# Kernel optimization log

Hardware: AMD Instinct MI355X
Metric: run time of the kernel (lower is better)

Reference implementation:

```python
import jax, jax.numpy as jnp
import numpy as np

N = 262144  # points
C = 256     # backbone_out_channels
K = 20      # semantic_num_classes
BN_EPS = 1e-3
EPS = 1e-8
IGNORE = -1


def setup_inputs() -> dict:
    key = jax.random.key(0)
    ks = jax.random.split(key, 12)
    feat = jax.random.normal(ks[0], (N, C), dtype=jnp.float32)
    coord = jax.random.normal(ks[1], (N, 3), dtype=jnp.float32)
    instance_centroid = jax.random.normal(ks[2], (N, 3), dtype=jnp.float32)
    segment = jax.random.randint(ks[3], (N,), 0, K, dtype=jnp.int32)
    instance = jax.random.randint(ks[4], (N,), 0, 1000, dtype=jnp.int32)
    # bias_head: Linear(C,C) -> BN1d(C) -> ReLU -> Linear(C,3)
    w1 = jax.random.normal(ks[5], (C, C), dtype=jnp.float32) * 0.02
    b1 = jnp.zeros((C,), dtype=jnp.float32)
    gamma = jnp.ones((C,), dtype=jnp.float32)
    beta = jnp.zeros((C,), dtype=jnp.float32)
    w2 = jax.random.normal(ks[6], (C, 3), dtype=jnp.float32) * 0.02
    b2 = jnp.zeros((3,), dtype=jnp.float32)
    # seg_head: Linear(C, K)
    ws = jax.random.normal(ks[7], (C, K), dtype=jnp.float32) * 0.02
    bs = jnp.zeros((K,), dtype=jnp.float32)
    return dict(feat=feat, coord=coord, instance_centroid=instance_centroid,
                segment=segment, instance=instance,
                w1=w1, b1=b1, gamma=gamma, beta=beta, w2=w2, b2=b2, ws=ws, bs=bs)


def reference(feat, coord, instance_centroid, segment, instance,
              w1, b1, gamma, beta, w2, b2, ws, bs):
    # bias head: Linear -> BatchNorm1d (training stats) -> ReLU -> Linear
    h = feat @ w1 + b1                                  # [N, C]
    mu = jnp.mean(h, axis=0)
    var = jnp.mean((h - mu) ** 2, axis=0)               # biased var (torch BN)
    h = (h - mu) * jax.lax.rsqrt(var + BN_EPS) * gamma + beta
    h = jax.nn.relu(h)
    bias_pred = h @ w2 + b2                             # [N, 3]

    logit_pred = feat @ ws + bs                         # [N, K]

    # semantic cross-entropy with ignore_index
    valid = segment != IGNORE
    tgt = jnp.where(valid, segment, 0)
    logp = jax.nn.log_softmax(logit_pred, axis=-1)
    nll = -jnp.take_along_axis(logp, tgt[:, None], axis=1)[:, 0]
    vf = valid.astype(logit_pred.dtype)
    seg_loss = jnp.sum(nll * vf) / (jnp.sum(vf) + EPS)

    # masked bias L1 loss
    mask = (instance != IGNORE).astype(bias_pred.dtype)
    bias_gt = instance_centroid - coord                 # [N, 3]
    bias_dist = jnp.sum(jnp.abs(bias_pred - bias_gt), axis=-1)
    msum = jnp.sum(mask) + EPS
    bias_l1_loss = jnp.sum(bias_dist * mask) / msum

    # masked cosine (direction) loss
    pred_n = bias_pred / (jnp.linalg.norm(bias_pred, axis=1, keepdims=True) + EPS)
    gt_n = bias_gt / (jnp.linalg.norm(bias_gt, axis=1, keepdims=True) + EPS)
    cos = -jnp.sum(pred_n * gt_n, axis=-1)
    bias_cosine_loss = jnp.sum(cos * mask) / msum

    loss = seg_loss + bias_l1_loss + bias_cosine_loss
    return jnp.stack([loss, seg_loss, bias_l1_loss, bias_cosine_loss])
```

## Files before the change

### kernel.cpp

```cpp
#include <hip/hip_runtime.h>
#include <cstdio>
#include <cstdint>

typedef unsigned int u32;
typedef unsigned short u16;
typedef short bf16x8 __attribute__((ext_vector_type(8)));
typedef float f32x4 __attribute__((ext_vector_type(4)));

#define NPTS 262144
#define CDIM 256
#define KCLS 20
#define NBLK 4096
#define NSLOT 256
#define LSLOT 256

#define OFF_WT    ((size_t)134217728)
#define OFF_AGGBN (OFF_WT + (size_t)163840)
#define OFF_AGGNL (OFF_AGGBN + (size_t)524288)
#define OFF_AGGL  (OFF_AGGNL + (size_t)2048)
#define OFF_AB    (OFF_AGGL + (size_t)4096)
#define WS_NEED   (OFF_AB + (size_t)2048)
#define MEMSET_OFF OFF_AGGBN
#define MEMSET_LEN ((size_t)(524288 + 2048 + 4096))

__device__ __forceinline__ u16 bf16rne(float x) {
    u32 u = __float_as_uint(x);
    u32 r = u + 0x7FFFu + ((u >> 16) & 1u);
    return (u16)(r >> 16);
}
__device__ __forceinline__ float bf2f(u16 b) {
    return __uint_as_float(((u32)b) << 16);
}

__global__ void k_prep(const float* __restrict__ w1, const float* __restrict__ wsm,
                       u16* __restrict__ Wt) {
    int k = blockIdx.x;
    int n = threadIdx.x;
    float v = 0.f;
    if (n < 256) v = w1[k * 256 + n];
    else if (n < 256 + KCLS) v = wsm[k * KCLS + (n - 256)];
    Wt[n * 256 + k] = bf16rne(v);
}

__global__ __launch_bounds__(256) void k_gemm(
    const float* __restrict__ feat, const float* __restrict__ b1,
    const float* __restrict__ bs, const int* __restrict__ segment,
    const u16* __restrict__ Wt, u16* __restrict__ h_out,
    float* __restrict__ aggBN, float* __restrict__ aggNLL)
{
    __shared__ uint4 smem4[3072];
    uint4* const As4 = smem4;
    uint4* const Bs4 = smem4 + 512;

    const int t = threadIdx.x;
    const int lane = t & 63;
    const int wv = t >> 6;
    const int q = lane >> 4;
    const int i16 = lane & 15;
    const int row0 = blockIdx.x * 64;
    const int slot = blockIdx.x & (NSLOT - 1);

    const f32x4 fz = {0.f, 0.f, 0.f, 0.f};
    f32x4 acc[4][4];
    f32x4 lacc[2];
#pragma unroll
    for (int r = 0; r < 4; ++r)
#pragma unroll
        for (int c = 0; c < 4; ++c) acc[r][c] = fz;
    lacc[0] = fz; lacc[1] = fz;

    const int sm = t >> 2;
    const int sq = t & 3;
    const float* fsrc = feat + (size_t)(row0 + sm) * 256 + sq * 8;
    const int wsl = sm ^ (sq << 2);
    const int As_slot0 = sq * 64 + wsl;
    const int As_slot1 = (sq + 4) * 64 + wsl;

    float4 f0 = *(const float4*)(fsrc);
    float4 f1 = *(const float4*)(fsrc + 4);
    float4 f2 = *(const float4*)(fsrc + 32);
    float4 f3 = *(const float4*)(fsrc + 36);

#pragma unroll 1
    for (int kc = 0; kc < 4; ++kc) {
        const int k0 = kc * 64;
        {
            uint4 pk;
            pk.x = (u32)bf16rne(f0.x) | ((u32)bf16rne(f0.y) << 16);
            pk.y = (u32)bf16rne(f0.z) | ((u32)bf16rne(f0.w) << 16);
            pk.z = (u32)bf16rne(f1.x) | ((u32)bf16rne(f1.y) << 16);
            pk.w = (u32)bf16rne(f1.z) | ((u32)bf16rne(f1.w) << 16);
            As4[As_slot0] = pk;
            pk.x = (u32)bf16rne(f2.x) | ((u32)bf16rne(f2.y) << 16);
            pk.y = (u32)bf16rne(f2.z) | ((u32)bf16rne(f2.w) << 16);
            pk.z = (u32)bf16rne(f3.x) | ((u32)bf16rne(f3.y) << 16);
            pk.w = (u32)bf16rne(f3.z) | ((u32)bf16rne(f3.w) << 16);
            As4[As_slot1] = pk;
        }
#pragma unroll
        for (int i = 0; i < 5; ++i) {
            const u16* src = Wt + (size_t)(i * 64 + lane) * 256 + k0 + wv * 8;
            u32* dst0 = (u32*)&Bs4[wv * 320 + i * 64];
            __builtin_amdgcn_global_load_lds(
                (const __attribute__((address_space(1))) u32*)src,
                (__attribute__((address_space(3))) u32*)dst0, 16, 0, 0);
            u32* dst1 = (u32*)&Bs4[(wv + 4) * 320 + i * 64];
            __builtin_amdgcn_global_load_lds(
                (const __attribute__((address_space(1))) u32*)(src + 32),
                (__attribute__((address_space(3))) u32*)dst1, 16, 0, 0);
        }
        __syncthreads();

        float4 fn0, fn1, fn2, fn3;
        if (kc < 3) {
            const float* p = fsrc + (kc + 1) * 64;
            fn0 = *(const float4*)(p);
            fn1 = *(const float4*)(p + 4);
            fn2 = *(const float4*)(p + 32);
            fn3 = *(const float4*)(p + 36);
        }

#pragma unroll
        for (int s = 0; s < 2; ++s) {
            const int kq = s * 4 + q;
            bf16x8 bfr[4], lbf[2], af[4], la;
#pragma unroll
            for (int c = 0; c < 4; ++c)
                bfr[c] = *(const bf16x8*)&Bs4[kq * 320 + wv * 64 + c * 16 + i16];
#pragma unroll
            for (int x = 0; x < 2; ++x)
                lbf[x] = *(const bf16x8*)&Bs4[kq * 320 + 256 + x * 16 + i16];
#pragma unroll
            for (int r = 0; r < 4; ++r)
                af[r] = *(const bf16x8*)&As4[kq * 64 + ((r * 16 + i16) ^ (q << 2))];
            la = *(const bf16x8*)&As4[kq * 64 + ((wv * 16 + i16) ^ (q << 2))];

#pragma unroll
            for (int r = 0; r < 4; ++r)
#pragma unroll
                for (int c = 0; c < 4; ++c)
                    acc[r][c] = __builtin_amdgcn_mfma_f32_16x16x32_bf16(af[r], bfr[c], acc[r][c], 0, 0, 0);
#pragma unroll
            for (int x = 0; x < 2; ++x)
                lacc[x] = __builtin_amdgcn_mfma_f32_16x16x32_bf16(la, lbf[x], lacc[x], 0, 0, 0);
        }
        __syncthreads();
        f0 = fn0; f1 = fn1; f2 = fn2; f3 = fn3;
    }

    float b1v[4];
#pragma unroll
    for (int c = 0; c < 4; ++c) b1v[c] = b1[wv * 64 + c * 16 + i16];
    float bsv0 = bs[i16];
    float bsv1 = (16 + i16 < KCLS) ? bs[16 + i16] : 0.f;

    float nllacc = 0.f, cntacc = 0.f;
#pragma unroll
    for (int j = 0; j < 4; ++j) {
        int rowr = row0 + wv * 16 + q * 4 + j;
        float l0 = lacc[0][j] + bsv0;
        float l1raw = lacc[1][j] + bsv1;
        float l1m = (i16 < 4) ? l1raw : -3.0e38f;
        float mx = fmaxf(l0, l1m);
#pragma unroll
        for (int d = 1; d < 16; d <<= 1) mx = fmaxf(mx, __shfl_xor(mx, d));
        float s = __expf(l0 - mx) + ((i16 < 4) ? __expf(l1raw - mx) : 0.f);
#pragma unroll
        for (int d = 1; d < 16; d <<= 1) s += __shfl_xor(s, d);
        int tg = segment[rowr];
        float v0 = __shfl(l0, (lane & 48) + (tg & 15));
        float v1 = __shfl(l1raw, (lane & 48) + ((tg - 16) & 15));
        float lt = (tg < 16) ? v0 : v1;
        if (i16 == 0 && tg >= 0) {
            nllacc += __logf(s) + mx - lt;
            cntacc += 1.f;
        }
    }
#pragma unroll
    for (int d = 1; d < 64; d <<= 1) {
        nllacc += __shfl_xor(nllacc, d);
        cntacc += __shfl_xor(cntacc, d);
    }
    if (lane == 0) {
        atomicAdd(aggNLL + slot * 2 + 0, nllacc);
        atomicAdd(aggNLL + slot * 2 + 1, cntacc);
    }

#pragma unroll
    for (int c = 0; c < 4; ++c) {
        float s1 = 0.f, s2 = 0.f;
#pragma unroll
        for (int r = 0; r < 4; ++r)
#pragma unroll
            for (int j = 0; j < 4; ++j) {
                float v = acc[r][c][j] + b1v[c];
                s1 += v; s2 = fmaf(v, v, s2);
            }
        s1 += __shfl_xor(s1, 16); s1 += __shfl_xor(s1, 32);
        s2 += __shfl_xor(s2, 16); s2 += __shfl_xor(s2, 32);
        if (q == 0) {
            int ch = wv * 64 + c * 16 + i16;
            atomicAdd(aggBN + slot * 512 + ch, s1);
            atomicAdd(aggBN + slot * 512 + 256 + ch, s2);
        }
    }

    u16* Ht = (u16*)smem4;
#pragma unroll
    for (int r = 0; r < 4; ++r)
#pragma unroll
        for (int c = 0; c < 4; ++c)
#pragma unroll
            for (int j = 0; j < 4; ++j) {
                float v = acc[r][c][j] + b1v[c];
                int rw = r * 16 + q * 4 + j;
                int cl = wv * 64 + c * 16 + i16;
                Ht[rw * 264 + cl] = bf16rne(v);
            }
    __syncthreads();
#pragma unroll
    for (int i = 0; i < 8; ++i) {
        int chunk = i * 256 + t;
        int m = chunk >> 5;
        int off = (chunk & 31) * 16;
        uint4 v = *(const uint4*)((const char*)smem4 + m * 528 + off);
        *(uint4*)((char*)h_out + (size_t)(row0 + m) * 512 + off) = v;
    }
}

__global__ void k_reduce(const float* __restrict__ gamma, const float* __restrict__ beta,
                         const float* __restrict__ aggBN,
                         float* __restrict__ Aarr, float* __restrict__ Barr) {
    int c = blockIdx.x;
    int l = threadIdx.x;
    float s1 = 0.f, s2 = 0.f;
#pragma unroll
    for (int i = 0; i < 4; ++i) {
        int s = l + i * 64;
        s1 += aggBN[s * 512 + c];
        s2 += aggBN[s * 512 + 256 + c];
    }
#pragma unroll
    for (int d = 1; d < 64; d <<= 1) {
        s1 += __shfl_xor(s1, d);
        s2 += __shfl_xor(s2, d);
    }
    if (l == 0) {
        const float inv = 1.f / (float)NPTS;
        float mu = s1 * inv;
        float var = fmaxf(s2 * inv - mu * mu, 0.f);
        float a = gamma[c] * rsqrtf(var + 1e-3f);
        Aarr[c] = a;
        Barr[c] = beta[c] - mu * a;
    }
}

__global__ __launch_bounds__(256) void k_loss(
    const u16* __restrict__ h, const float* __restrict__ Aarr, const float* __restrict__ Barr,
    const float* __restrict__ w2, const float* __restrict__ b2,
    const float* __restrict__ coord, const float* __restrict__ cent,
    const int* __restrict__ inst, float* __restrict__ aggL)
{
    __shared__ u16 hs[64 * 264];
    __shared__ float w2s[768];
    __shared__ float As_l[256], Bs_l[256];
    __shared__ float bp[4][16][4];
    __shared__ float red[12];

    const int t = threadIdx.x;
    const int lane = t & 63;
    const int wv = t >> 6;
    const int q = lane >> 4;
    const int i16 = lane & 15;
    const int row0 = blockIdx.x * 64;

#pragma unroll
    for (int i = 0; i < 8; ++i) {
        int chunk = i * 256 + t;
        int m = chunk >> 5;
        int off = (chunk & 31) * 16;
        *(uint4*)((char*)hs + m * 528 + off) =
            *(const uint4*)((const char*)h + (size_t)(row0 + m) * 512 + off);
    }
    if (t < 256) { As_l[t] = Aarr[t]; Bs_l[t] = Barr[t]; }
    for (int i = t; i < 768; i += 256) w2s[i] = w2[i];
    __syncthreads();

    bf16x8 wfr[8];
#pragma unroll
    for (int kc = 0; kc < 8; ++kc) {
        bf16x8 f;
#pragma unroll
        for (int j = 0; j < 8; ++j) {
            int k = kc * 32 + q * 8 + j;
            float v = (i16 < 3) ? w2s[k * 3 + i16] : 0.f;
            ((u16*)&f)[j] = bf16rne(v);
        }
        wfr[kc] = f;
    }
    float b2x = b2[0], b2y = b2[1], b2z = b2[2];

    const f32x4 fz = {0.f, 0.f, 0.f, 0.f};
    f32x4 c = fz;
#pragma unroll
    for (int kc = 0; kc < 8; ++kc) {
        bf16x8 hf = *(const bf16x8*)(hs + (wv * 16 + i16) * 264 + kc * 32 + q * 8);
        float4 a0 = *(const float4*)(As_l + kc * 32 + q * 8);
        float4 a1 = *(const float4*)(As_l + kc * 32 + q * 8 + 4);
        float4 b0 = *(const float4*)(Bs_l + kc * 32 + q * 8);
        float4 b1 = *(const float4*)(Bs_l + kc * 32 + q * 8 + 4);
        float av[8] = {a0.x, a0.y, a0.z, a0.w, a1.x, a1.y, a1.z, a1.w};
        float bv[8] = {b0.x, b0.y, b0.z, b0.w, b1.x, b1.y, b1.z, b1.w};
        bf16x8 hn;
#pragma unroll
        for (int j = 0; j < 8; ++j) {
            float x = fmaxf(fmaf(bf2f(((const u16*)&hf)[j]), av[j], bv[j]), 0.f);
            ((u16*)&hn)[j] = bf16rne(x);
        }
        c = __builtin_amdgcn_mfma_f32_16x16x32_bf16(hn, wfr[kc], c, 0, 0, 0);
    }

    if (i16 < 3) {
#pragma unroll
        for (int j = 0; j < 4; ++j) bp[wv][q * 4 + j][i16] = c[j];
    }
    float l1a = 0.f, cosa = 0.f, ma = 0.f;
    if (lane < 16) {
        int row = row0 + wv * 16 + lane;
        float4 P = *(const float4*)bp[wv][lane];
        float bpx = P.x + b2x, bpy = P.y + b2y, bpz = P.z + b2z;
        const float* cp = coord + (size_t)row * 3;
        const float* ip = cent + (size_t)row * 3;
        float gx = ip[0] - cp[0], gy = ip[1] - cp[1], gz = ip[2] - cp[2];
        float mk = (inst[row] != -1) ? 1.f : 0.f;
        float l1 = fabsf(bpx - gx) + fabsf(bpy - gy) + fabsf(bpz - gz);
        float np = sqrtf(fmaf(bpx, bpx, fmaf(bpy, bpy, bpz * bpz)));
        float ng = sqrtf(fmaf(gx, gx, fmaf(gy, gy, gz * gz)));
        float dp = fmaf(bpx, gx, fmaf(bpy, gy, bpz * gz));
        float cosv = -dp / ((np + 1e-8f) * (ng + 1e-8f));
        l1a = l1 * mk;
        cosa = cosv * mk;
        ma = mk;
    }
#pragma unroll
    for (int d = 1; d < 64; d <<= 1) {
        l1a += __shfl_xor(l1a, d);
        cosa += __shfl_xor(cosa, d);
        ma += __shfl_xor(ma, d);
    }
    if (lane == 0) { red[wv] = l1a; red[4 + wv] = cosa; red[8 + wv] = ma; }
    __syncthreads();
    if (t == 0) {
        int slot = blockIdx.x & (LSLOT - 1);
        atomicAdd(aggL + slot * 4 + 0, red[0] + red[1] + red[2] + red[3]);
        atomicAdd(aggL + slot * 4 + 1, red[4] + red[5] + red[6] + red[7]);
        atomicAdd(aggL + slot * 4 + 2, red[8] + red[9] + red[10] + red[11]);
    }
}

__global__ void k_final(const float* __restrict__ aggNLL, const float* __restrict__ aggL,
                        float* __restrict__ out) {
    int lane = threadIdx.x;
    float nll = 0.f, cnt = 0.f, l1 = 0.f, cs = 0.f, mk = 0.f;
#pragma unroll
    for (int i = 0; i < 4; ++i) {
        int s = lane + i * 64;
        nll += aggNLL[s * 2 + 0];
        cnt += aggNLL[s * 2 + 1];
        l1 += aggL[s * 4 + 0];
        cs += aggL[s * 4 + 1];
        mk += aggL[s * 4 + 2];
    }
#pragma unroll
    for (int d = 1; d < 64; d <<= 1) {
        nll += __shfl_xor(nll, d);
        cnt += __shfl_xor(cnt, d);
        l1 += __shfl_xor(l1, d);
        cs += __shfl_xor(cs, d);
        mk += __shfl_xor(mk, d);
    }
    if (lane == 0) {
        float seg = nll / (cnt + 1e-8f);
        float l1l = l1 / (mk + 1e-8f);
        float csl = cs / (mk + 1e-8f);
        out[0] = seg + l1l + csl;
        out[1] = seg;
        out[2] = l1l;
        out[3] = csl;
    }
}

extern "C" void kernel_launch(void* const* d_in, const int* in_sizes, int n_in,
                              void* d_out, int out_size, void* d_ws, size_t ws_size,
                              hipStream_t stream) {
    const float* feat   = (const float*)d_in[0];
    const float* coord  = (const float*)d_in[1];
    const float* cent   = (const float*)d_in[2];
    const int* segment  = (const int*)d_in[3];
    const int* inst     = (const int*)d_in[4];
    const float* w1     = (const float*)d_in[5];
    const float* b1     = (const float*)d_in[6];
    const float* gamma  = (const float*)d_in[7];
    const float* beta   = (const float*)d_in[8];
    const float* w2     = (const float*)d_in[9];
    const float* b2     = (const float*)d_in[10];
    const float* wsm    = (const float*)d_in[11];
    const float* bs     = (const float*)d_in[12];
    float* out = (float*)d_out;

    char* wsb = (char*)d_ws;
    u16* h_ws    = (u16*)wsb;
    u16* Wt      = (u16*)(wsb + OFF_WT);
    float* aggBN = (float*)(wsb + OFF_AGGBN);
    float* aggNL = (float*)(wsb + OFF_AGGNL);
    float* aggL  = (float*)(wsb + OFF_AGGL);
    float* Aarr  = (float*)(wsb + OFF_AB);
    float* Barr  = Aarr + 256;

    if (ws_size < WS_NEED)
        fprintf(stderr, "kernel_launch: ws_size=%zu < needed %zu — WILL CORRUPT\n",
                ws_size, (size_t)WS_NEED);

    hipMemsetAsync(wsb + MEMSET_OFF, 0, MEMSET_LEN, stream);
    k_prep<<<256, 320, 0, stream>>>(w1, wsm, Wt);
    k_gemm<<<NBLK, 256, 0, stream>>>(feat, b1, bs, segment, Wt, h_ws, aggBN, aggNL);
    k_reduce<<<256, 64, 0, stream>>>(gamma, beta, aggBN, Aarr, Barr);
    k_loss<<<4096, 256, 0, stream>>>(h_ws, Aarr, Barr, w2, b2, coord, cent, inst, aggL);
    k_final<<<1, 64, 0, stream>>>(aggNL, aggL, out);
}
```

Baseline: 510.3 us.

## Pre-pack weights in k-chunked layout, shrink GEMM LDS, precompute bf16 w2 fragments

The prep kernel now writes W1/Ws in a k-chunk-major packed layout so each async global-to-LDS load reads contiguous 16-byte chunks. It also writes a bf16 transposed w2 so the loss kernel loads its MFMA fragments straight from global memory instead of converting them per block. The segmentation-head weight columns are no longer staged in LDS; they are read directly from global memory, which cuts GEMM LDS from 48KB to 40KB. Both kernels get launch_bounds occupancy hints of 4, which frees LDS for more resident blocks but adds global-load latency inside the MFMA loop.

Result: slower. 563.1 us (+10.3%).

```diff
diff --git a/kernel.cpp b/kernel.cpp
--- a/kernel.cpp
+++ b/kernel.cpp
@@ -15,7 +15,8 @@
 #define LSLOT 256
 
 #define OFF_WT    ((size_t)134217728)
-#define OFF_AGGBN (OFF_WT + (size_t)163840)
+#define OFF_W2T   (OFF_WT + (size_t)163840)
+#define OFF_AGGBN (OFF_W2T + (size_t)8192)
 #define OFF_AGGNL (OFF_AGGBN + (size_t)524288)
 #define OFF_AGGL  (OFF_AGGNL + (size_t)2048)
 #define OFF_AB    (OFF_AGGL + (size_t)4096)
@@ -33,22 +34,24 @@
 }
 
 __global__ void k_prep(const float* __restrict__ w1, const float* __restrict__ wsm,
-                       u16* __restrict__ Wt) {
+                       const float* __restrict__ w2,
+                       u16* __restrict__ Wt2, u16* __restrict__ w2t) {
     int k = blockIdx.x;
     int n = threadIdx.x;
     float v = 0.f;
     if (n < 256) v = w1[k * 256 + n];
     else if (n < 256 + KCLS) v = wsm[k * KCLS + (n - 256)];
-    Wt[n * 256 + k] = bf16rne(v);
-}
-
-__global__ __launch_bounds__(256) void k_gemm(
+    Wt2[((size_t)(k >> 3) * 320 + n) * 8 + (k & 7)] = bf16rne(v);
+    if (n < 16) w2t[n * 256 + k] = bf16rne((n < 3) ? w2[k * 3 + n] : 0.f);
+}
+
+__global__ __launch_bounds__(256, 4) void k_gemm(
     const float* __restrict__ feat, const float* __restrict__ b1,
     const float* __restrict__ bs, const int* __restrict__ segment,
-    const u16* __restrict__ Wt, u16* __restrict__ h_out,
+    const u16* __restrict__ Wt2, u16* __restrict__ h_out,
     float* __restrict__ aggBN, float* __restrict__ aggNLL)
 {
-    __shared__ uint4 smem4[3072];
+    __shared__ uint4 smem4[2560];
     uint4* const As4 = smem4;
     uint4* const Bs4 = smem4 + 512;
 
@@ -83,7 +86,6 @@
 
 #pragma unroll 1
     for (int kc = 0; kc < 4; ++kc) {
-        const int k0 = kc * 64;
         {
             uint4 pk;
             pk.x = (u32)bf16rne(f0.x) | ((u32)bf16rne(f0.y) << 16);
@@ -98,15 +100,16 @@
             As4[As_slot1] = pk;
         }
 #pragma unroll
-        for (int i = 0; i < 5; ++i) {
-            const u16* src = Wt + (size_t)(i * 64 + lane) * 256 + k0 + wv * 8;
-            u32* dst0 = (u32*)&Bs4[wv * 320 + i * 64];
+        for (int i = 0; i < 4; ++i) {
+            const u16* src0 = Wt2 + ((size_t)(kc * 8 + wv) * 320 + i * 64 + lane) * 8;
+            u32* dst0 = (u32*)&Bs4[wv * 256 + i * 64];
             __builtin_amdgcn_global_load_lds(
-                (const __attribute__((address_space(1))) u32*)src,
+                (const __attribute__((address_space(1))) u32*)src0,
                 (__attribute__((address_space(3))) u32*)dst0, 16, 0, 0);
-            u32* dst1 = (u32*)&Bs4[(wv + 4) * 320 + i * 64];
+            const u16* src1 = Wt2 + ((size_t)(kc * 8 + wv + 4) * 320 + i * 64 + lane) * 8;
+            u32* dst1 = (u32*)&Bs4[(wv + 4) * 256 + i * 64];
             __builtin_amdgcn_global_load_lds(
-                (const __attribute__((address_space(1))) u32*)(src + 32),
+                (const __attribute__((address_space(1))) u32*)src1,
                 (__attribute__((address_space(3))) u32*)dst1, 16, 0, 0);
         }
         __syncthreads();
@@ -123,13 +126,15 @@
 #pragma unroll
         for (int s = 0; s < 2; ++s) {
             const int kq = s * 4 + q;
-            bf16x8 bfr[4], lbf[2], af[4], la;
+            bf16x8 lbf[2];
+#pragma unroll
+            for (int x = 0; x < 2; ++x)
+                lbf[x] = *(const bf16x8*)(Wt2 +
+                    ((size_t)(kc * 8 + kq) * 320 + 256 + x * 16 + i16) * 8);
+            bf16x8 bfr[4], af[4], la;
 #pragma unroll
             for (int c = 0; c < 4; ++c)
-                bfr[c] = *(const bf16x8*)&Bs4[kq * 320 + wv * 64 + c * 16 + i16];
-#pragma unroll
-            for (int x = 0; x < 2; ++x)
-                lbf[x] = *(const bf16x8*)&Bs4[kq * 320 + 256 + x * 16 + i16];
+                bfr[c] = *(const bf16x8*)&Bs4[kq * 256 + wv * 64 + c * 16 + i16];
 #pragma unroll
             for (int r = 0; r < 4; ++r)
                 af[r] = *(const bf16x8*)&As4[kq * 64 + ((r * 16 + i16) ^ (q << 2))];
@@ -255,14 +260,13 @@
     }
 }
 
-__global__ __launch_bounds__(256) void k_loss(
+__global__ __launch_bounds__(256, 4) void k_loss(
     const u16* __restrict__ h, const float* __restrict__ Aarr, const float* __restrict__ Barr,
-    const float* __restrict__ w2, const float* __restrict__ b2,
+    const u16* __restrict__ w2t, const float* __restrict__ b2,
     const float* __restrict__ coord, const float* __restrict__ cent,
     const int* __restrict__ inst, float* __restrict__ aggL)
 {
     __shared__ u16 hs[64 * 264];
-    __shared__ float w2s[768];
     __shared__ float As_l[256], Bs_l[256];
     __shared__ float bp[4][16][4];
     __shared__ float red[12];
@@ -283,22 +287,13 @@
             *(const uint4*)((const char*)h + (size_t)(row0 + m) * 512 + off);
     }
     if (t < 256) { As_l[t] = Aarr[t]; Bs_l[t] = Barr[t]; }
-    for (int i = t; i < 768; i += 256) w2s[i] = w2[i];
+
+    bf16x8 wfr[8];
+#pragma unroll
+    for (int kc = 0; kc < 8; ++kc)
+        wfr[kc] = *(const bf16x8*)(w2t + (size_t)i16 * 256 + kc * 32 + q * 8);
+    float b2x = b2[0], b2y = b2[1], b2z = b2[2];
     __syncthreads();
-
-    bf16x8 wfr[8];
-#pragma unroll
-    for (int kc = 0; kc < 8; ++kc) {
-        bf16x8 f;
-#pragma unroll
-        for (int j = 0; j < 8; ++j) {
-            int k = kc * 32 + q * 8 + j;
-            float v = (i16 < 3) ? w2s[k * 3 + i16] : 0.f;
-            ((u16*)&f)[j] = bf16rne(v);
-        }
-        wfr[kc] = f;
-    }
-    float b2x = b2[0], b2y = b2[1], b2z = b2[2];
 
     const f32x4 fz = {0.f, 0.f, 0.f, 0.f};
     f32x4 c = fz;
@@ -410,7 +405,8 @@
 
     char* wsb = (char*)d_ws;
     u16* h_ws    = (u16*)wsb;
-    u16* Wt      = (u16*)(wsb + OFF_WT);
+    u16* Wt2     = (u16*)(wsb + OFF_WT);
+    u16* w2t     = (u16*)(wsb + OFF_W2T);
     float* aggBN = (float*)(wsb + OFF_AGGBN);
     float* aggNL = (float*)(wsb + OFF_AGGNL);
     float* aggL  = (float*)(wsb + OFF_AGGL);
@@ -422,9 +418,9 @@
                 ws_size, (size_t)WS_NEED);
 
     hipMemsetAsync(wsb + MEMSET_OFF, 0, MEMSET_LEN, stream);
-    k_prep<<<256, 320, 0, stream>>>(w1, wsm, Wt);
-    k_gemm<<<NBLK, 256, 0, stream>>>(feat, b1, bs, segment, Wt, h_ws, aggBN, aggNL);
+    k_prep<<<256, 320, 0, stream>>>(w1, wsm, w2, Wt2, w2t);
+    k_gemm<<<NBLK, 256, 0, stream>>>(feat, b1, bs, segment, Wt2, h_ws, aggBN, aggNL);
     k_reduce<<<256, 64, 0, stream>>>(gamma, beta, aggBN, Aarr, Barr);
-    k_loss<<<4096, 256, 0, stream>>>(h_ws, Aarr, Barr, w2, b2, coord, cent, inst, aggL);
+    k_loss<<<4096, 256, 0, stream>>>(h_ws, Aarr, Barr, w2t, b2, coord, cent, inst, aggL);
     k_final<<<1, 64, 0, stream>>>(aggNL, aggL, out);
 }
```
